# Performance work log

Measured on AMD Instinct MI355X. Metric: run time of the kernel, lower is better.

Reference implementation:

```python
import jax, jax.numpy as jnp
import numpy as np

NUM_HEADS = 16
HEAD_DIM = 64
TAU = 0.07
EPS = 1e-12  # torch F.normalize eps


def setup_inputs() -> dict:
    key = jax.random.key(0)
    ks = jax.random.split(key, 12)
    B, L, D = 4, 2048, 1024
    s = 1.0 / np.sqrt(D)
    inp = {
        'q': jax.random.normal(ks[0], (B, L, D), jnp.float32),
        'k': jax.random.normal(ks[1], (B, L, D), jnp.float32),
        'v': jax.random.normal(ks[2], (B, L, D), jnp.float32),
        'Wq': jax.random.normal(ks[3], (D, D), jnp.float32) * s,
        'bq': jax.random.normal(ks[4], (D,), jnp.float32) * 0.01,
        'Wk': jax.random.normal(ks[5], (D, D), jnp.float32) * s,
        'bk': jax.random.normal(ks[6], (D,), jnp.float32) * 0.01,
        'Wv': jax.random.normal(ks[7], (D, D), jnp.float32) * s,
        'bv': jax.random.normal(ks[8], (D,), jnp.float32) * 0.01,
        'Wo': jax.random.normal(ks[9], (D, D), jnp.float32) * s,
        'bo': jax.random.normal(ks[10], (D,), jnp.float32) * 0.01,
    }
    return inp


def _split(x):
    b, l, d = x.shape
    return x.reshape(b, l, NUM_HEADS, HEAD_DIM).transpose(0, 2, 1, 3)  # [b,h,l,dh]


def _l2norm(x):
    n = jnp.sqrt(jnp.sum(x * x, axis=-1, keepdims=True))
    return x / jnp.maximum(n, EPS)


def reference(q, k, v, Wq, bq, Wk, bk, Wv, bv, Wo, bo):
    # Linear projections (torch Linear: y = x @ W.T + b)
    qh = _l2norm(_split(q @ Wq.T + bq))
    kh = _l2norm(_split(k @ Wk.T + bk))
    vh = _split(v @ Wv.T + bv)
    scores = jnp.einsum('bhqd,bhkd->bhqk', qh, kh) / max(TAU, 1e-6)
    attn = jax.nn.softmax(scores, axis=-1)  # dropout = identity in eval
    out = jnp.einsum('bhqk,bhkd->bhqd', attn, vh)
    b, h, l, dh = out.shape
    merged = out.transpose(0, 2, 1, 3).reshape(b, l, h * dh)
    return merged @ Wo.T + bo
```

## Files before the change

kernel.cpp:

```cpp
#include <hip/hip_runtime.h>

#define BB 4
#define LL 2048
#define DD 1024
#define NH 16
#define DH 64
#define MM (BB*LL)

typedef _Float16 half8 __attribute__((ext_vector_type(8)));
typedef _Float16 half4 __attribute__((ext_vector_type(4)));
typedef _Float16 half2 __attribute__((ext_vector_type(2)));
typedef float floatx4 __attribute__((ext_vector_type(4)));
typedef float floatx16 __attribute__((ext_vector_type(16)));
typedef unsigned uint4v __attribute__((ext_vector_type(4)));

__device__ __forceinline__ void gload_lds16(const void* g, void* l) {
    __builtin_amdgcn_global_load_lds((const __attribute__((address_space(1))) void*)g,
                                     (__attribute__((address_space(3))) void*)l,
                                     16, 0, 0);
}

__device__ __forceinline__ floatx4 mfma16(half8 a, half8 b, floatx4 c) {
    return __builtin_amdgcn_mfma_f32_16x16x32_f16(a, b, c, 0, 0, 0);
}

__device__ __forceinline__ floatx16 mfma32(half8 a, half8 b, floatx16 c) {
    return __builtin_amdgcn_mfma_f32_32x32x16_f16(a, b, c, 0, 0, 0);
}

__device__ __forceinline__ unsigned pkh(float a, float b) {
    return __builtin_bit_cast(unsigned, __builtin_amdgcn_cvt_pkrtz(a, b));
}

__global__ __launch_bounds__(256) void cvt_all(const float* __restrict__ q,
                                               const float* __restrict__ k,
                                               const float* __restrict__ v,
                                               const float* __restrict__ Wq,
                                               const float* __restrict__ Wk,
                                               const float* __restrict__ Wv,
                                               const float* __restrict__ Wo,
                                               _Float16* __restrict__ dst) {
    const int BIG = 8192;
    const int SML = 1024;
    const size_t NQKV = (size_t)MM * DD;
    const size_t NW = (size_t)DD * DD;
    int b = blockIdx.x;
    const float* src;
    size_t off;
    int lb;
    if (b < 3 * BIG) {
        int t = b / BIG;
        src = t == 0 ? q : (t == 1 ? k : v);
        off = (size_t)t * NQKV;
        lb = b - t * BIG;
    } else {
        int t = (b - 3 * BIG) / SML;
        src = t == 0 ? Wq : (t == 1 ? Wk : (t == 2 ? Wv : Wo));
        off = 3 * NQKV + (size_t)t * NW;
        lb = b - 3 * BIG - t * SML;
    }
    size_t i = (size_t)lb * 256 + threadIdx.x;
    float4 f = ((const float4*)src)[i];
    half4 h;
    h[0] = (_Float16)f.x; h[1] = (_Float16)f.y;
    h[2] = (_Float16)f.z; h[3] = (_Float16)f.w;
    ((half4*)(dst + off))[i] = h;
}

__global__ __launch_bounds__(256) void gemm_qkv(const _Float16* __restrict__ qkv16,
                                                const _Float16* __restrict__ wq,
                                                const _Float16* __restrict__ wk,
                                                const _Float16* __restrict__ wv,
                                                const float* __restrict__ bq,
                                                const float* __restrict__ bk,
                                                const float* __restrict__ bv,
                                                _Float16* __restrict__ Qp,
                                                _Float16* __restrict__ Kp,
                                                _Float16* __restrict__ VtG) {
    const int K = 1024;
    __shared__ _Float16 As[2][128 * 32];
    __shared__ _Float16 Bs[2][128 * 32];

    int tid = threadIdx.x;
    int wave = tid >> 6, lane = tid & 63;
    int quad = lane >> 4, l15 = lane & 15;
    int wrow = (wave >> 1) * 64, wcol = (wave & 1) * 64;
    int bx = blockIdx.x;
    int which = bx >> 3;
    int m0 = blockIdx.y * 128;
    int n0 = (bx & 7) * 128;

    const _Float16* A = qkv16 + (size_t)which * ((size_t)MM * DD);
    const _Float16* W = which == 0 ? wq : (which == 1 ? wk : wv);
    const float* bias = which == 0 ? bq : (which == 1 ? bk : bv);

    floatx4 acc[4][4] = {};

    int srow = tid >> 2, sseg = tid & 3;
    const _Float16* Ag0 = A + (size_t)(m0 + srow) * K + sseg * 8;
    const _Float16* Ag1 = Ag0 + (size_t)64 * K;
    const _Float16* Bg0 = W + (size_t)(n0 + srow) * K + sseg * 8;
    const _Float16* Bg1 = Bg0 + (size_t)64 * K;
    int lo0 = tid * 16, lo1 = (256 + tid) * 16;

    gload_lds16(Ag0, (char*)As[0] + lo0);
    gload_lds16(Ag1, (char*)As[0] + lo1);
    gload_lds16(Bg0, (char*)Bs[0] + lo0);
    gload_lds16(Bg1, (char*)Bs[0] + lo1);
    __syncthreads();

    for (int kt = 0; kt < K; kt += 32) {
        int cur = (kt >> 5) & 1;
        if (kt + 32 < K) {
            gload_lds16(Ag0 + kt + 32, (char*)As[cur ^ 1] + lo0);
            gload_lds16(Ag1 + kt + 32, (char*)As[cur ^ 1] + lo1);
            gload_lds16(Bg0 + kt + 32, (char*)Bs[cur ^ 1] + lo0);
            gload_lds16(Bg1 + kt + 32, (char*)Bs[cur ^ 1] + lo1);
        }

        half8 af[4], bf[4];
#pragma unroll
        for (int i = 0; i < 4; i++)
            af[i] = *(half8*)&As[cur][(wrow + i * 16 + l15) * 32 + quad * 8];
#pragma unroll
        for (int j = 0; j < 4; j++)
            bf[j] = *(half8*)&Bs[cur][(wcol + j * 16 + l15) * 32 + quad * 8];
#pragma unroll
        for (int i = 0; i < 4; i++)
#pragma unroll
            for (int j = 0; j < 4; j++)
                acc[i][j] = mfma16(af[i], bf[j], acc[i][j]);

        __syncthreads();
    }

#pragma unroll
    for (int j = 0; j < 4; j++) {
        float bv_ = bias[n0 + wcol + j * 16 + l15];
#pragma unroll
        for (int i = 0; i < 4; i++)
#pragma unroll
            for (int r = 0; r < 4; r++) acc[i][j][r] += bv_;
    }

    if (which < 2) {
        _Float16* C = which == 0 ? Qp : Kp;
#pragma unroll
        for (int i = 0; i < 4; i++) {
#pragma unroll
            for (int r = 0; r < 4; r++) {
                float s = 0.f;
#pragma unroll
                for (int j = 0; j < 4; j++) s += acc[i][j][r] * acc[i][j][r];
                s += __shfl_xor(s, 1);
                s += __shfl_xor(s, 2);
                s += __shfl_xor(s, 4);
                s += __shfl_xor(s, 8);
                float inv = 1.0f / fmaxf(sqrtf(s), 1e-12f);
                int row = m0 + wrow + i * 16 + quad * 4 + r;
#pragma unroll
                for (int j = 0; j < 4; j++) {
                    int col = n0 + wcol + j * 16 + l15;
                    C[(size_t)row * DD + col] = (_Float16)(acc[i][j][r] * inv);
                }
            }
        }
    } else {
#pragma unroll
        for (int j = 0; j < 4; j++) {
            int col = n0 + wcol + j * 16 + l15;
#pragma unroll
            for (int i = 0; i < 4; i++) {
#pragma unroll
                for (int r = 0; r < 4; r++) {
                    int row = m0 + wrow + i * 16 + quad * 4 + r;
                    int b = row >> 11, l = row & 2047;
                    VtG[((size_t)((b << 10) + col)) * LL + l] = (_Float16)acc[i][j][r];
                }
            }
        }
    }
}

__global__ __launch_bounds__(256) void gemm_out(const _Float16* __restrict__ A,
                                                const _Float16* __restrict__ W,
                                                const float* __restrict__ bias,
                                                float* __restrict__ C) {
    const int K = 1024, N = 1024;
    __shared__ _Float16 As[2][128 * 32];
    __shared__ _Float16 Bs[2][128 * 32];

    int tid = threadIdx.x;
    int wave = tid >> 6, lane = tid & 63;
    int quad = lane >> 4, l15 = lane & 15;
    int wrow = (wave >> 1) * 64, wcol = (wave & 1) * 64;
    int m0 = blockIdx.y * 128;
    int n0 = blockIdx.x * 128;

    floatx4 acc[4][4] = {};

    int srow = tid >> 2, sseg = tid & 3;
    const _Float16* Ag0 = A + (size_t)(m0 + srow) * K + sseg * 8;
    const _Float16* Ag1 = Ag0 + (size_t)64 * K;
    const _Float16* Bg0 = W + (size_t)(n0 + srow) * K + sseg * 8;
    const _Float16* Bg1 = Bg0 + (size_t)64 * K;
    int lo0 = tid * 16, lo1 = (256 + tid) * 16;

    gload_lds16(Ag0, (char*)As[0] + lo0);
    gload_lds16(Ag1, (char*)As[0] + lo1);
    gload_lds16(Bg0, (char*)Bs[0] + lo0);
    gload_lds16(Bg1, (char*)Bs[0] + lo1);
    __syncthreads();

    for (int kt = 0; kt < K; kt += 32) {
        int cur = (kt >> 5) & 1;
        if (kt + 32 < K) {
            gload_lds16(Ag0 + kt + 32, (char*)As[cur ^ 1] + lo0);
            gload_lds16(Ag1 + kt + 32, (char*)As[cur ^ 1] + lo1);
            gload_lds16(Bg0 + kt + 32, (char*)Bs[cur ^ 1] + lo0);
            gload_lds16(Bg1 + kt + 32, (char*)Bs[cur ^ 1] + lo1);
        }

        half8 af[4], bf[4];
#pragma unroll
        for (int i = 0; i < 4; i++)
            af[i] = *(half8*)&As[cur][(wrow + i * 16 + l15) * 32 + quad * 8];
#pragma unroll
        for (int j = 0; j < 4; j++)
            bf[j] = *(half8*)&Bs[cur][(wcol + j * 16 + l15) * 32 + quad * 8];
#pragma unroll
        for (int i = 0; i < 4; i++)
#pragma unroll
            for (int j = 0; j < 4; j++)
                acc[i][j] = mfma16(af[i], bf[j], acc[i][j]);

        __syncthreads();
    }

#pragma unroll
    for (int j = 0; j < 4; j++) {
        int col = n0 + wcol + j * 16 + l15;
        float bv = bias[col];
#pragma unroll
        for (int i = 0; i < 4; i++) {
#pragma unroll
            for (int r = 0; r < 4; r++) {
                int row = m0 + wrow + i * 16 + quad * 4 + r;
                C[(size_t)row * N + col] = acc[i][j][r] + bv;
            }
        }
    }
}

__global__ __launch_bounds__(256) void attn_k(const _Float16* __restrict__ Q,
                                              const _Float16* __restrict__ K,
                                              const _Float16* __restrict__ VtG,
                                              _Float16* __restrict__ Mg) {
    __shared__ _Float16 Ks[2][64 * 64];
    __shared__ _Float16 Vt[2][64 * 64];
    __shared__ float lsum[128];

    const float C2 = 20.60992915555662f;
    const float OFF = 6.0f;

    int tid = threadIdx.x, wave = tid >> 6, lane = tid & 63;
    int l31 = lane & 31, hi = lane >> 5;

    int hw = blockIdx.x + blockIdx.y * gridDim.x;
    int logical = (hw & 7) * 128 + (hw >> 3);
    int bh = logical >> 4;
    int q0 = (logical & 15) * 128;

    int b = bh >> 4, h = bh & 15;
    size_t rowBase = (size_t)b * LL;
    int colBase = h * 64;
    int wq = wave * 32;
    int xorv = l31 & 7;

    half8 qf[4];
    const _Float16* qp = Q + (rowBase + q0 + wq + l31) * DD + colBase + hi * 8;
#pragma unroll
    for (int d = 0; d < 4; d++) qf[d] = *(const half8*)(qp + d * 16);

    const _Float16* kg[2];
    const _Float16* vg[2];
    int ldso[2];
#pragma unroll
    for (int p = 0; p < 2; p++) {
        int s = p * 256 + tid;
        int r = s >> 3, cp = s & 7;
        int cs = cp ^ (r & 7);
        kg[p] = K + (rowBase + r) * DD + colBase + cs * 8;
        vg[p] = VtG + ((size_t)bh * 64 + r) * LL + cs * 8;
        ldso[p] = s * 16;
    }

    floatx16 oacc[2] = {};
    float fsum = 0.f;

    gload_lds16(kg[0], (char*)Ks[0] + ldso[0]);
    gload_lds16(kg[1], (char*)Ks[0] + ldso[1]);
    gload_lds16(vg[0], (char*)Vt[0] + ldso[0]);
    gload_lds16(vg[1], (char*)Vt[0] + ldso[1]);
    kg[0] += 64 * DD; kg[1] += 64 * DD; vg[0] += 64; vg[1] += 64;
    __syncthreads();

#pragma unroll 2
    for (int kt = 0; kt < LL / 64; kt++) {
        int cur = kt & 1;
        if (kt + 1 < LL / 64) {
            gload_lds16(kg[0], (char*)Ks[cur ^ 1] + ldso[0]);
            gload_lds16(kg[1], (char*)Ks[cur ^ 1] + ldso[1]);
            gload_lds16(vg[0], (char*)Vt[cur ^ 1] + ldso[0]);
            gload_lds16(vg[1], (char*)Vt[cur ^ 1] + ldso[1]);
            kg[0] += 64 * DD; kg[1] += 64 * DD; vg[0] += 64; vg[1] += 64;
        }
        const char* kb_ = (const char*)Ks[cur];
        const char* vb_ = (const char*)Vt[cur];

#pragma unroll
        for (int c = 0; c < 2; c++) {
            floatx16 st = {};
            __builtin_amdgcn_s_setprio(1);
#pragma unroll
            for (int d = 0; d < 4; d++) {
                half8 kf = *(const half8*)(kb_ + c * 4096 + l31 * 128 +
                                           (((d * 2 + hi) ^ xorv) * 16));
                st = mfma32(kf, qf[d], st);
            }
            __builtin_amdgcn_s_setprio(0);

            float e[16];
#pragma unroll
            for (int r = 0; r < 16; r++)
                e[r] = __builtin_amdgcn_exp2f(st[r] * C2 - OFF);

            float s0 = (e[0] + e[1]) + (e[2] + e[3]);
            float s1 = (e[4] + e[5]) + (e[6] + e[7]);
            float s2 = (e[8] + e[9]) + (e[10] + e[11]);
            float s3 = (e[12] + e[13]) + (e[14] + e[15]);
            fsum += (s0 + s1) + (s2 + s3);

            half8 pf[2];
#pragma unroll
            for (int sl = 0; sl < 2; sl++) {
                int bse = sl * 8;
                unsigned a = pkh(e[bse + 0], e[bse + 1]);
                unsigned cc = pkh(e[bse + 2], e[bse + 3]);
                unsigned bb = pkh(e[bse + 4], e[bse + 5]);
                unsigned dd = pkh(e[bse + 6], e[bse + 7]);
                auto r1 = __builtin_amdgcn_permlane32_swap(a, bb, false, false);
                auto r2 = __builtin_amdgcn_permlane32_swap(cc, dd, false, false);
                uint4v u;
                u[0] = (unsigned)r1[0]; u[1] = (unsigned)r2[0];
                u[2] = (unsigned)r1[1]; u[3] = (unsigned)r2[1];
                pf[sl] = __builtin_bit_cast(half8, u);
            }

            __builtin_amdgcn_s_setprio(1);
#pragma unroll
            for (int jb = 0; jb < 2; jb++) {
#pragma unroll
                for (int sl = 0; sl < 2; sl++) {
                    half8 vf = *(const half8*)(vb_ + jb * 4096 + l31 * 128 +
                                               (((c * 4 + sl * 2 + hi) ^ xorv) * 16));
                    oacc[jb] = mfma32(pf[sl], vf, oacc[jb]);
                }
            }
            __builtin_amdgcn_s_setprio(0);
        }

        __syncthreads();
    }

    fsum += __shfl_xor(fsum, 32);
    lsum[wq + l31] = fsum;
    __syncthreads();

    float inv[16];
#pragma unroll
    for (int r = 0; r < 16; r++) {
        int crow = (r & 3) + 8 * (r >> 2) + 4 * hi;
        inv[r] = 1.0f / lsum[wq + crow];
    }

    _Float16* mp = Mg + (rowBase + q0 + wq) * DD + colBase + l31;
#pragma unroll
    for (int jb = 0; jb < 2; jb++) {
#pragma unroll
        for (int r = 0; r < 16; r++) {
            int crow = (r & 3) + 8 * (r >> 2) + 4 * hi;
            mp[(size_t)crow * DD + jb * 32] = (_Float16)(oacc[jb][r] * inv[r]);
        }
    }
}

extern "C" void kernel_launch(void* const* d_in, const int* in_sizes, int n_in,
                              void* d_out, int out_size, void* d_ws, size_t ws_size,
                              hipStream_t stream) {
    (void)in_sizes; (void)n_in; (void)out_size; (void)ws_size;
    const float* q  = (const float*)d_in[0];
    const float* k  = (const float*)d_in[1];
    const float* v  = (const float*)d_in[2];
    const float* Wq = (const float*)d_in[3];
    const float* bq = (const float*)d_in[4];
    const float* Wk = (const float*)d_in[5];
    const float* bk = (const float*)d_in[6];
    const float* Wv = (const float*)d_in[7];
    const float* bv = (const float*)d_in[8];
    const float* Wo = (const float*)d_in[9];
    const float* bo = (const float*)d_in[10];

    const size_t NQKV = (size_t)MM * DD;
    const size_t NW = (size_t)DD * DD;

    _Float16* q16  = (_Float16*)d_ws;
    _Float16* k16  = q16 + NQKV;
    _Float16* v16  = k16 + NQKV;
    _Float16* wq16 = v16 + NQKV;
    _Float16* wk16 = wq16 + NW;
    _Float16* wv16 = wk16 + NW;
    _Float16* wo16 = wv16 + NW;
    _Float16* Qp   = wo16 + NW;
    _Float16* Kp   = Qp + NQKV;
    _Float16* VtG  = Kp + NQKV;
    _Float16* Mg   = VtG + NQKV;
    (void)k16; (void)v16;

    cvt_all<<<dim3(3 * 8192 + 4 * 1024), dim3(256), 0, stream>>>(q, k, v, Wq, Wk, Wv, Wo, q16);

    gemm_qkv<<<dim3(24, MM / 128), dim3(256), 0, stream>>>(q16, wq16, wk16, wv16,
                                                           bq, bk, bv, Qp, Kp, VtG);

    attn_k<<<dim3(LL / 128, BB * NH), dim3(256), 0, stream>>>(Qp, Kp, VtG, Mg);

    gemm_out<<<dim3(1024 / 128, MM / 128), dim3(256), 0, stream>>>(Mg, wo16, bo, (float*)d_out);
}
```

Measured before the change: 373.9 us.

## Split attention keys across waves with per-wave pipelines and LDS reduction

The attention kernel now processes 64 query rows per block, and each of the four waves handles a disjoint quarter of the key sequence with its own double-buffered LDS tiles. Waves wait with s_waitcnt instead of block-wide barriers inside the loop. Each K/V fragment is reused across two 32-row query groups. Partial outputs and row sums are reduced through LDS by wave 0 at the end. This removes per-iteration __syncthreads and doubles the grid, at the cost of more LDS (about 65 KB, which lowers occupancy), more Q/K/V global traffic per output, and a serial epilogue on one wave.

```diff
diff --git a/kernel.cpp b/kernel.cpp
--- a/kernel.cpp
+++ b/kernel.cpp
@@ -256,9 +256,7 @@
                                               const _Float16* __restrict__ K,
                                               const _Float16* __restrict__ VtG,
                                               _Float16* __restrict__ Mg) {
-    __shared__ _Float16 Ks[2][64 * 64];
-    __shared__ _Float16 Vt[2][64 * 64];
-    __shared__ float lsum[128];
+    __shared__ __attribute__((aligned(16))) char LDSBUF[66560];
 
     const float C2 = 20.60992915555662f;
     const float OFF = 6.0f;
@@ -267,81 +265,105 @@
     int l31 = lane & 31, hi = lane >> 5;
 
     int hw = blockIdx.x + blockIdx.y * gridDim.x;
-    int logical = (hw & 7) * 128 + (hw >> 3);
-    int bh = logical >> 4;
-    int q0 = (logical & 15) * 128;
+    int logical = (hw & 7) * 256 + (hw >> 3);
+    int bh = logical >> 5;
+    int q0 = (logical & 31) * 64;
 
     int b = bh >> 4, h = bh & 15;
     size_t rowBase = (size_t)b * LL;
     int colBase = h * 64;
-    int wq = wave * 32;
+    int k0 = wave * 512;
     int xorv = l31 & 7;
 
-    half8 qf[4];
-    const _Float16* qp = Q + (rowBase + q0 + wq + l31) * DD + colBase + hi * 8;
-#pragma unroll
-    for (int d = 0; d < 4; d++) qf[d] = *(const half8*)(qp + d * 16);
-
-    const _Float16* kg[2];
-    const _Float16* vg[2];
-    int ldso[2];
-#pragma unroll
-    for (int p = 0; p < 2; p++) {
-        int s = p * 256 + tid;
-        int r = s >> 3, cp = s & 7;
-        int cs = cp ^ (r & 7);
-        kg[p] = K + (rowBase + r) * DD + colBase + cs * 8;
-        vg[p] = VtG + ((size_t)bh * 64 + r) * LL + cs * 8;
-        ldso[p] = s * 16;
-    }
-
-    floatx16 oacc[2] = {};
-    float fsum = 0.f;
-
-    gload_lds16(kg[0], (char*)Ks[0] + ldso[0]);
-    gload_lds16(kg[1], (char*)Ks[0] + ldso[1]);
-    gload_lds16(vg[0], (char*)Vt[0] + ldso[0]);
-    gload_lds16(vg[1], (char*)Vt[0] + ldso[1]);
-    kg[0] += 64 * DD; kg[1] += 64 * DD; vg[0] += 64; vg[1] += 64;
-    __syncthreads();
+    half8 qfA[4], qfB[4];
+    {
+        const _Float16* qpA = Q + (rowBase + q0 + l31) * DD + colBase + hi * 8;
+        const _Float16* qpB = qpA + (size_t)32 * DD;
+#pragma unroll
+        for (int d = 0; d < 4; d++) {
+            qfA[d] = *(const half8*)(qpA + d * 16);
+            qfB[d] = *(const half8*)(qpB + d * 16);
+        }
+    }
+
+    const _Float16* kg[4];
+    const _Float16* vg[4];
+#pragma unroll
+    for (int p = 0; p < 4; p++) {
+        int s = p * 64 + lane;
+        int kr = s >> 3, kseg = (s & 7) ^ (kr & 7);
+        kg[p] = K + (rowBase + k0 + kr) * DD + colBase + kseg * 8;
+        int vr = s >> 2, vseg = (s & 3) ^ (vr & 3);
+        vg[p] = VtG + ((size_t)bh * 64 + vr) * LL + k0 + vseg * 8;
+    }
+    char* kl = LDSBUF + wave * 8192;
+    char* vl = LDSBUF + 32768 + wave * 8192;
+
+    floatx16 oaccA[2] = {}, oaccB[2] = {};
+    float fsA = 0.f, fsB = 0.f;
+
+#pragma unroll
+    for (int p = 0; p < 4; p++) {
+        gload_lds16(kg[p], kl + p * 1024 + lane * 16);
+        gload_lds16(vg[p], vl + p * 1024 + lane * 16);
+        kg[p] += (size_t)32 * DD;
+        vg[p] += 32;
+    }
 
 #pragma unroll 2
-    for (int kt = 0; kt < LL / 64; kt++) {
-        int cur = kt & 1;
-        if (kt + 1 < LL / 64) {
-            gload_lds16(kg[0], (char*)Ks[cur ^ 1] + ldso[0]);
-            gload_lds16(kg[1], (char*)Ks[cur ^ 1] + ldso[1]);
-            gload_lds16(vg[0], (char*)Vt[cur ^ 1] + ldso[0]);
-            gload_lds16(vg[1], (char*)Vt[cur ^ 1] + ldso[1]);
-            kg[0] += 64 * DD; kg[1] += 64 * DD; vg[0] += 64; vg[1] += 64;
-        }
-        const char* kb_ = (const char*)Ks[cur];
-        const char* vb_ = (const char*)Vt[cur];
-
-#pragma unroll
-        for (int c = 0; c < 2; c++) {
-            floatx16 st = {};
-            __builtin_amdgcn_s_setprio(1);
-#pragma unroll
-            for (int d = 0; d < 4; d++) {
-                half8 kf = *(const half8*)(kb_ + c * 4096 + l31 * 128 +
-                                           (((d * 2 + hi) ^ xorv) * 16));
-                st = mfma32(kf, qf[d], st);
-            }
-            __builtin_amdgcn_s_setprio(0);
-
+    for (int t = 0; t < 16; t++) {
+        int cur = t & 1;
+        if (t < 15) {
+            char* kld = kl + (cur ^ 1) * 4096;
+            char* vld = vl + (cur ^ 1) * 4096;
+#pragma unroll
+            for (int p = 0; p < 4; p++) {
+                gload_lds16(kg[p], kld + p * 1024 + lane * 16);
+                gload_lds16(vg[p], vld + p * 1024 + lane * 16);
+                kg[p] += (size_t)32 * DD;
+                vg[p] += 32;
+            }
+            asm volatile("s_waitcnt vmcnt(8)" ::: "memory");
+        } else {
+            asm volatile("s_waitcnt vmcnt(0)" ::: "memory");
+        }
+        __builtin_amdgcn_sched_barrier(0);
+
+        const char* kb = kl + cur * 4096;
+        const char* vb = vl + cur * 4096;
+
+        half8 kf[4];
+#pragma unroll
+        for (int d = 0; d < 4; d++)
+            kf[d] = *(const half8*)(kb + l31 * 128 + (((d * 2 + hi) ^ xorv) * 16));
+        floatx16 stA = {}, stB = {};
+        __builtin_amdgcn_s_setprio(1);
+#pragma unroll
+        for (int d = 0; d < 4; d++) {
+            stA = mfma32(kf[d], qfA[d], stA);
+            stB = mfma32(kf[d], qfB[d], stB);
+        }
+        __builtin_amdgcn_s_setprio(0);
+
+        half8 vf[2][2];
+#pragma unroll
+        for (int jb = 0; jb < 2; jb++)
+#pragma unroll
+            for (int sl = 0; sl < 2; sl++)
+                vf[jb][sl] = *(const half8*)(vb + (jb * 32 + l31) * 64 +
+                                             (((sl * 2 + hi) ^ (l31 & 3)) * 16));
+
+        half8 pfA[2], pfB[2];
+        {
             float e[16];
 #pragma unroll
             for (int r = 0; r < 16; r++)
-                e[r] = __builtin_amdgcn_exp2f(st[r] * C2 - OFF);
-
+                e[r] = __builtin_amdgcn_exp2f(stA[r] * C2 - OFF);
             float s0 = (e[0] + e[1]) + (e[2] + e[3]);
             float s1 = (e[4] + e[5]) + (e[6] + e[7]);
             float s2 = (e[8] + e[9]) + (e[10] + e[11]);
             float s3 = (e[12] + e[13]) + (e[14] + e[15]);
-            fsum += (s0 + s1) + (s2 + s3);
-
-            half8 pf[2];
+            fsA += (s0 + s1) + (s2 + s3);
 #pragma unroll
             for (int sl = 0; sl < 2; sl++) {
                 int bse = sl * 8;
@@ -354,44 +376,107 @@
                 uint4v u;
                 u[0] = (unsigned)r1[0]; u[1] = (unsigned)r2[0];
                 u[2] = (unsigned)r1[1]; u[3] = (unsigned)r2[1];
-                pf[sl] = __builtin_bit_cast(half8, u);
-            }
-
-            __builtin_amdgcn_s_setprio(1);
-#pragma unroll
-            for (int jb = 0; jb < 2; jb++) {
-#pragma unroll
-                for (int sl = 0; sl < 2; sl++) {
-                    half8 vf = *(const half8*)(vb_ + jb * 4096 + l31 * 128 +
-                                               (((c * 4 + sl * 2 + hi) ^ xorv) * 16));
-                    oacc[jb] = mfma32(pf[sl], vf, oacc[jb]);
+                pfA[sl] = __builtin_bit_cast(half8, u);
+            }
+        }
+        {
+            float e[16];
+#pragma unroll
+            for (int r = 0; r < 16; r++)
+                e[r] = __builtin_amdgcn_exp2f(stB[r] * C2 - OFF);
+            float s0 = (e[0] + e[1]) + (e[2] + e[3]);
+            float s1 = (e[4] + e[5]) + (e[6] + e[7]);
+            float s2 = (e[8] + e[9]) + (e[10] + e[11]);
+            float s3 = (e[12] + e[13]) + (e[14] + e[15]);
+            fsB += (s0 + s1) + (s2 + s3);
+#pragma unroll
+            for (int sl = 0; sl < 2; sl++) {
+                int bse = sl * 8;
+                unsigned a = pkh(e[bse + 0], e[bse + 1]);
+                unsigned cc = pkh(e[bse + 2], e[bse + 3]);
+                unsigned bb = pkh(e[bse + 4], e[bse + 5]);
+                unsigned dd = pkh(e[bse + 6], e[bse + 7]);
+                auto r1 = __builtin_amdgcn_permlane32_swap(a, bb, false, false);
+                auto r2 = __builtin_amdgcn_permlane32_swap(cc, dd, false, false);
+                uint4v u;
+                u[0] = (unsigned)r1[0]; u[1] = (unsigned)r2[0];
+                u[2] = (unsigned)r1[1]; u[3] = (unsigned)r2[1];
+                pfB[sl] = __builtin_bit_cast(half8, u);
+            }
+        }
+
+        __builtin_amdgcn_s_setprio(1);
+#pragma unroll
+        for (int jb = 0; jb < 2; jb++)
+#pragma unroll
+            for (int sl = 0; sl < 2; sl++) {
+                oaccA[jb] = mfma32(pfA[sl], vf[jb][sl], oaccA[jb]);
+                oaccB[jb] = mfma32(pfB[sl], vf[jb][sl], oaccB[jb]);
+            }
+        __builtin_amdgcn_s_setprio(0);
+    }
+
+    fsA += __shfl_xor(fsA, 32);
+    fsB += __shfl_xor(fsB, 32);
+    float* lsumPf = (float*)(LDSBUF + 65536);
+    if (lane < 32) {
+        lsumPf[wave * 64 + l31] = fsA;
+        lsumPf[wave * 64 + 32 + l31] = fsB;
+    }
+
+    __syncthreads();
+
+    if (wave != 0) {
+        char* cb = LDSBUF + (wave - 1) * 16384;
+#pragma unroll
+        for (int jb = 0; jb < 2; jb++)
+#pragma unroll
+            for (int q4 = 0; q4 < 4; q4++) {
+                floatx4 va, vb2;
+#pragma unroll
+                for (int r = 0; r < 4; r++) {
+                    va[r] = oaccA[jb][q4 * 4 + r];
+                    vb2[r] = oaccB[jb][q4 * 4 + r];
                 }
-            }
-            __builtin_amdgcn_s_setprio(0);
-        }
-
-        __syncthreads();
-    }
-
-    fsum += __shfl_xor(fsum, 32);
-    lsum[wq + l31] = fsum;
+                *(floatx4*)(cb + (jb * 4 + q4) * 1024 + lane * 16) = va;
+                *(floatx4*)(cb + ((2 + jb) * 4 + q4) * 1024 + lane * 16) = vb2;
+            }
+    }
     __syncthreads();
 
-    float inv[16];
-#pragma unroll
-    for (int r = 0; r < 16; r++) {
-        int crow = (r & 3) + 8 * (r >> 2) + 4 * hi;
-        inv[r] = 1.0f / lsum[wq + crow];
-    }
-
-    _Float16* mp = Mg + (rowBase + q0 + wq) * DD + colBase + l31;
-#pragma unroll
-    for (int jb = 0; jb < 2; jb++) {
-#pragma unroll
-        for (int r = 0; r < 16; r++) {
-            int crow = (r & 3) + 8 * (r >> 2) + 4 * hi;
-            mp[(size_t)crow * DD + jb * 32] = (_Float16)(oacc[jb][r] * inv[r]);
-        }
+    if (wave == 0) {
+#pragma unroll
+        for (int w1 = 0; w1 < 3; w1++) {
+            char* cb = LDSBUF + w1 * 16384;
+#pragma unroll
+            for (int jb = 0; jb < 2; jb++)
+#pragma unroll
+                for (int q4 = 0; q4 < 4; q4++) {
+                    floatx4 va = *(floatx4*)(cb + (jb * 4 + q4) * 1024 + lane * 16);
+                    floatx4 vb2 = *(floatx4*)(cb + ((2 + jb) * 4 + q4) * 1024 + lane * 16);
+#pragma unroll
+                    for (int r = 0; r < 4; r++) {
+                        oaccA[jb][q4 * 4 + r] += va[r];
+                        oaccB[jb][q4 * 4 + r] += vb2[r];
+                    }
+                }
+        }
+        float tq = lsumPf[0 * 64 + hi * 32 + l31] + lsumPf[1 * 64 + hi * 32 + l31] +
+                   lsumPf[2 * 64 + hi * 32 + l31] + lsumPf[3 * 64 + hi * 32 + l31];
+        float invq = 1.0f / tq;
+
+#pragma unroll
+        for (int g = 0; g < 2; g++)
+#pragma unroll
+            for (int jb = 0; jb < 2; jb++)
+#pragma unroll
+                for (int r = 0; r < 16; r++) {
+                    int crow = (r & 3) + 8 * (r >> 2) + 4 * hi;
+                    float iv = __shfl(invq, g * 32 + crow);
+                    float val = (g ? oaccB : oaccA)[jb][r] * iv;
+                    Mg[(rowBase + q0 + g * 32 + crow) * DD + colBase + jb * 32 + l31] =
+                        (_Float16)val;
+                }
     }
 }
 
@@ -432,7 +517,7 @@
     gemm_qkv<<<dim3(24, MM / 128), dim3(256), 0, stream>>>(q16, wq16, wk16, wv16,
                                                            bq, bk, bv, Qp, Kp, VtG);
 
-    attn_k<<<dim3(LL / 128, BB * NH), dim3(256), 0, stream>>>(Qp, Kp, VtG, Mg);
+    attn_k<<<dim3(32, 64), dim3(256), 0, stream>>>(Qp, Kp, VtG, Mg);
 
     gemm_out<<<dim3(1024 / 128, MM / 128), dim3(256), 0, stream>>>(Mg, wo16, bo, (float*)d_out);
 }
```

After: 377.6 us. No clear change (+1.0%).
